# Optimization experiments

Measured on AMD Instinct MI355X. Metric: run time of the kernel, lower is better.

## Reference

```python
import jax, jax.numpy as jnp
import numpy as np

NUM_EXPERTS = 4
HIDDEN = 768
INTER = 192  # expert_inter; gate_up projects to 2*INTER
TOKENS = 131072


def setup_inputs() -> dict:
    key = jax.random.key(0)
    k1, k2, k3, k4 = jax.random.split(key, 4)
    hidden = jax.random.normal(k1, (TOKENS, HIDDEN), dtype=jnp.float32)
    expert_ids = jax.random.randint(k2, (TOKENS,), 0, NUM_EXPERTS, dtype=jnp.int64)
    gate_up = jax.random.normal(k3, (NUM_EXPERTS, HIDDEN, 2 * INTER), dtype=jnp.float32) * 0.02
    down = jax.random.normal(k4, (NUM_EXPERTS, INTER, HIDDEN), dtype=jnp.float32) * 0.02
    return {"hidden": hidden, "expert_ids": expert_ids, "gate_up": gate_up, "down": down}


def reference(hidden, expert_ids, gate_up, down):
    # Math-equivalent to scatter -> per-expert SwiGLU MLP -> gather back:
    # for each token t with expert e = expert_ids[t]:
    #   out[t] = (silu(x_t @ gate_up[e][:, :F]) * (x_t @ gate_up[e][:, F:])) @ down[e]
    # With E=4 (small), compute per-expert dense and select via one-hot; this is
    # jit-friendly (static shapes) and exactly matches the per-token math.
    E = gate_up.shape[0]
    F = down.shape[1]
    onehot = (expert_ids[None, :] == jnp.arange(E)[:, None]).astype(hidden.dtype)  # [E, T]
    gu = jnp.einsum('th,ehf->etf', hidden, gate_up)      # [E, T, 2F]
    gate, up = gu[..., :F], gu[..., F:]                  # [E, T, F]
    act = jax.nn.silu(gate) * up                         # SwiGLU
    out = jnp.einsum('etf,efh,et->th', act, down, onehot)  # select token's own expert
    return out
```

## Files before the change

### kernel.cpp

```cpp
#include <hip/hip_runtime.h>
#include <hip/hip_bf16.h>

#define NE 4
#define HD 768
#define F2 384
#define F1 192
#define NT 131072
#define TT 128

typedef __attribute__((ext_vector_type(8))) short bf16x8;
typedef __attribute__((ext_vector_type(4))) float f32x4;
typedef __attribute__((ext_vector_type(4))) unsigned int u32x4;

#define SMEM_BYTES 123392
#define LTOK 122880u

#define WS_BUCKET_OFF 256
#define WS_B1IMG_OFF (WS_BUCKET_OFF + NE*NT*4)
#define WS_DNIMG_OFF (WS_B1IMG_OFF + NE*24*24576)

__device__ __forceinline__ unsigned short f2bf(float x) {
    unsigned int u = __float_as_uint(x);
    return (unsigned short)((u + 0x7fffu + ((u >> 16) & 1u)) >> 16);
}
__device__ __forceinline__ unsigned int pk2(float a, float b) {
    unsigned int ua = __float_as_uint(a), ub = __float_as_uint(b);
    unsigned int lo = (ua + 0x7fffu + ((ua >> 16) & 1u)) >> 16;
    unsigned int hi = (ub + 0x7fffu + ((ub >> 16) & 1u)) & 0xffff0000u;
    return lo | hi;
}
#define GLL(srcp, ldsoff) \
    __builtin_amdgcn_global_load_lds((const __attribute__((address_space(1))) void*)(srcp), \
        (__attribute__((address_space(3))) void*)(smem + (ldsoff)), 16, 0, 0)

__global__ void route_kernel(const int* __restrict__ ids, int* __restrict__ counts,
                             int* __restrict__ bucket) {
    __shared__ int lc[NE];
    __shared__ int lb[NE];
    int tid = threadIdx.x;
    if (tid < NE) lc[tid] = 0;
    __syncthreads();
    int t = blockIdx.x * blockDim.x + tid;
    int e = ids[t];
    int rank = atomicAdd(&lc[e], 1);
    __syncthreads();
    if (tid < NE) lb[tid] = atomicAdd(&counts[tid], lc[tid]);
    __syncthreads();
    bucket[e * NT + lb[e] + rank] = t;
}

__global__ void b1img_kernel(const float* __restrict__ gu, unsigned short* __restrict__ b1img) {
    int idx = blockIdx.x * 256 + threadIdx.x;
    int L = idx % 1536;
    int es = idx / 1536;
    int kstep = es % 24, e = es / 24;
    int colp = L >> 3, slot = L & 7;
    int v = slot ^ (colp & 7);
    int tc = colp * 2 + (v >> 2);
    int kb = kstep * 32 + (v & 3) * 8;
    const float* src = gu + ((size_t)(e * HD + kb)) * F2 + tc;
    unsigned short o[8];
    #pragma unroll
    for (int j = 0; j < 8; ++j) o[j] = f2bf(src[(size_t)j * F2]);
    *(bf16x8*)(b1img + ((size_t)idx) * 8) = *(const bf16x8*)o;
}

__global__ void dnimg_kernel(const float* __restrict__ dn, unsigned short* __restrict__ dnimg) {
    int idx = blockIdx.x * 256 + threadIdx.x;
    int L = idx % 1536;
    int r = idx / 1536;
    int kt = r % 6; r /= 6;
    int half = r & 1; int e = r >> 1;
    int colp = L >> 3, slot = L & 7;
    int v = slot ^ (colp & 7);
    int tc = colp * 2 + (v >> 2);
    int kb = kt * 32 + (v & 3) * 8;
    const float* src = dn + ((size_t)(e * F1 + kb)) * HD + half * 384 + tc;
    unsigned short o[8];
    #pragma unroll
    for (int j = 0; j < 8; ++j) o[j] = f2bf(src[(size_t)j * HD]);
    *(bf16x8*)(dnimg + ((size_t)idx) * 8) = *(const bf16x8*)o;
}

__global__ __launch_bounds__(512, 1)
void moe_kernel(const float* __restrict__ hidden, const int* __restrict__ counts,
                const int* __restrict__ bucket, const unsigned short* __restrict__ b1img,
                const unsigned short* __restrict__ dnimg, float* __restrict__ out)
{
    extern __shared__ __align__(16) unsigned char smem[];
    const unsigned LAo[2] = {0u, 8192u};
    const unsigned LBo[4] = {16384u, 40960u, 65536u, 90112u};
    const unsigned LCo[3] = {49152u, 73728u, 98304u};
    const unsigned LACT = 0u;

    int rem = blockIdx.x, e, n_e = 0;
    for (e = 0; e < NE; ++e) {
        n_e = counts[e];
        int ntiles = (n_e + TT - 1) >> 7;
        if (rem < ntiles) break;
        rem -= ntiles;
    }
    if (e >= NE) return;
    int t0 = rem << 7;

    int tid = threadIdx.x;
    int lane = tid & 63;
    int w = tid >> 6;
    int rw64 = (w >> 2) << 6;
    int cq = w & 3;
    int lg = lane >> 4;
    int l16 = lane & 15;

    int* tokp = (int*)(smem + LTOK);
    if (tid < TT) {
        int idx = t0 + tid; if (idx >= n_e) idx = n_e - 1;
        tokp[tid] = bucket[e * NT + idx];
    }
    __syncthreads();

    int arow = tid >> 2, kq = tid & 3;
    const float* aptr = hidden + (size_t)tokp[arow] * HD + kq * 8;
    unsigned awb = (unsigned)((tid >> 3) * 128 +
                   (((kq + ((arow & 1) << 2)) ^ ((tid >> 3) & 7)) << 4));

    const unsigned short* gls  = b1img + (size_t)e * 24 * 12288 + (w * 3) * 512 + lane * 8;
    const unsigned short* gls2 = dnimg + (size_t)e * 12 * 12288 + (w * 3) * 512 + lane * 8;
    unsigned gld = (unsigned)(w * 3) * 1024u;

    unsigned laneoff = (unsigned)(((l16 >> 1) << 7) +
                       (((lg + ((l16 & 1) << 2)) ^ (l16 >> 1)) << 4));
    unsigned arb[4], brb[6], b2rb[6];
    #pragma unroll
    for (int mt = 0; mt < 4; ++mt)
        arb[mt] = (unsigned)((rw64 + mt * 16) * 64) + laneoff;
    #pragma unroll
    for (int nt = 0; nt < 6; ++nt) {
        int tcb = (nt < 3) ? (cq * 48 + nt * 16) : (192 + cq * 48 + (nt - 3) * 16);
        brb[nt] = (unsigned)(tcb * 64) + laneoff;
        b2rb[nt] = (unsigned)((cq * 96 + nt * 16) * 64) + laneoff;
    }

    f32x4 avb[4][2];
    const f32x4 fzero = {0.f, 0.f, 0.f, 0.f};
    f32x4 acc[4][6];
    #pragma unroll
    for (int mt = 0; mt < 4; ++mt)
        #pragma unroll
        for (int nt = 0; nt < 6; ++nt) acc[mt][nt] = fzero;

    {
        #pragma unroll
        for (int i = 0; i < 3; ++i) GLL(gls + i * 512, LBo[0] + gld + i * 1024u);
        #pragma unroll
        for (int j = 0; j < 4; ++j) {
            const f32x4* p = (const f32x4*)(aptr + j * 32);
            avb[j][0] = p[0]; avb[j][1] = p[1];
        }
        #pragma unroll
        for (int i = 0; i < 3; ++i) GLL(gls + 12288 + i * 512, LBo[1] + gld + i * 1024u);
        #pragma unroll
        for (int i = 0; i < 3; ++i) GLL(gls + 2 * 12288 + i * 512, LBo[2] + gld + i * 1024u);
        u32x4 vv = {pk2(avb[0][0].x,avb[0][0].y), pk2(avb[0][0].z,avb[0][0].w),
                    pk2(avb[0][1].x,avb[0][1].y), pk2(avb[0][1].z,avb[0][1].w)};
        *(u32x4*)(smem + LAo[0] + awb) = vv;
        asm volatile("s_waitcnt vmcnt(14) lgkmcnt(0)");
        __builtin_amdgcn_s_barrier();
        __builtin_amdgcn_sched_barrier(0);
    }

    #pragma unroll
    for (int g = 0; g < 24; ++g) {
        if (g < 21) {
            #pragma unroll
            for (int i = 0; i < 3; ++i)
                GLL(gls + (size_t)(g + 3) * 12288 + i * 512, LBo[(g + 3) & 3] + gld + i * 1024u);
        }
        if (g < 20) {
            const f32x4* p = (const f32x4*)(aptr + (g + 4) * 32);
            avb[g & 3][0] = p[0]; avb[g & 3][1] = p[1];
        }

        bf16x8 Af[4];
        #pragma unroll
        for (int mt = 0; mt < 4; ++mt)
            Af[mt] = *(const bf16x8*)(smem + LAo[g & 1] + arb[mt]);
        __builtin_amdgcn_s_setprio(1);
        #pragma unroll
        for (int nt = 0; nt < 6; ++nt) {
            bf16x8 Bf = *(const bf16x8*)(smem + LBo[g & 3] + brb[nt]);
            #pragma unroll
            for (int mt = 0; mt < 4; ++mt)
                acc[mt][nt] = __builtin_amdgcn_mfma_f32_16x16x32_bf16(Af[mt], Bf, acc[mt][nt], 0, 0, 0);
        }
        __builtin_amdgcn_s_setprio(0);

        if (g < 23) {
            f32x4 a0 = avb[(g + 1) & 3][0], a1 = avb[(g + 1) & 3][1];
            u32x4 vv = {pk2(a0.x,a0.y), pk2(a0.z,a0.w), pk2(a1.x,a1.y), pk2(a1.z,a1.w)};
            *(u32x4*)(smem + LAo[(g + 1) & 1] + awb) = vv;
            if (g == 0)       asm volatile("s_waitcnt vmcnt(8) lgkmcnt(0)");
            else if (g == 1)  asm volatile("s_waitcnt vmcnt(10) lgkmcnt(0)");
            else if (g <= 19) asm volatile("s_waitcnt vmcnt(12) lgkmcnt(0)");
            else if (g == 20) asm volatile("s_waitcnt vmcnt(10) lgkmcnt(0)");
            else if (g == 21) asm volatile("s_waitcnt vmcnt(5) lgkmcnt(0)");
            else              asm volatile("s_waitcnt vmcnt(0) lgkmcnt(0)");
            __builtin_amdgcn_s_barrier();
            __builtin_amdgcn_sched_barrier(0);
        }
    }

    asm volatile("s_waitcnt vmcnt(0) lgkmcnt(0)");
    __builtin_amdgcn_s_barrier();
    __builtin_amdgcn_sched_barrier(0);

    #pragma unroll
    for (int i = 0; i < 3; ++i) GLL(gls2 + i * 512, LCo[0] + gld + i * 1024u);
    #pragma unroll
    for (int i = 0; i < 3; ++i) GLL(gls2 + 12288 + i * 512, LCo[1] + gld + i * 1024u);

    #pragma unroll
    for (int mt = 0; mt < 4; ++mt)
        #pragma unroll
        for (int nt = 0; nt < 3; ++nt)
            #pragma unroll
            for (int p = 0; p < 4; ++p) {
                float g = acc[mt][nt][p];
                float u = acc[mt][nt + 3][p];
                float s = g / (1.f + __expf(-g));
                int row = rw64 + mt * 16 + 4 * lg + p;
                int f = cq * 48 + nt * 16 + l16;
                int c = f >> 3;
                unsigned b = (unsigned)(LACT + row * 384 + (((c & 24) | ((c & 7) ^ (row & 7))) << 4) + (f & 7) * 2);
                *(unsigned short*)(smem + b) = f2bf(s * u);
            }
    asm volatile("s_waitcnt vmcnt(3) lgkmcnt(0)");
    __builtin_amdgcn_s_barrier();
    __builtin_amdgcn_sched_barrier(0);

    #pragma unroll
    for (int half = 0; half < 2; ++half) {
        f32x4 c2[4][6];
        #pragma unroll
        for (int mt = 0; mt < 4; ++mt)
            #pragma unroll
            for (int nt = 0; nt < 6; ++nt) c2[mt][nt] = fzero;

        #pragma unroll
        for (int kt = 0; kt < 6; ++kt) {
            const int s = half * 6 + kt;
            if (s < 10) {
                #pragma unroll
                for (int i = 0; i < 3; ++i)
                    GLL(gls2 + (size_t)(s + 2) * 12288 + i * 512, LCo[(s + 2) % 3] + gld + i * 1024u);
            }

            int c = kt * 4 + lg;
            unsigned a2sl = (unsigned)(((c & 24) | ((c & 7) ^ (l16 & 7))) << 4);
            bf16x8 A2[4];
            #pragma unroll
            for (int mt = 0; mt < 4; ++mt)
                A2[mt] = *(const bf16x8*)(smem + LACT + (rw64 + mt * 16 + l16) * 384 + a2sl);
            __builtin_amdgcn_s_setprio(1);
            #pragma unroll
            for (int nt = 0; nt < 6; ++nt) {
                bf16x8 B2f = *(const bf16x8*)(smem + LCo[s % 3] + b2rb[nt]);
                #pragma unroll
                for (int mt = 0; mt < 4; ++mt)
                    c2[mt][nt] = __builtin_amdgcn_mfma_f32_16x16x32_bf16(A2[mt], B2f, c2[mt][nt], 0, 0, 0);
            }
            __builtin_amdgcn_s_setprio(0);

            if (s < 11) {
                if (s < 10) asm volatile("s_waitcnt vmcnt(3) lgkmcnt(0)");
                else        asm volatile("s_waitcnt vmcnt(0) lgkmcnt(0)");
                __builtin_amdgcn_s_barrier();
                __builtin_amdgcn_sched_barrier(0);
            }
        }

        #pragma unroll
        for (int mt = 0; mt < 4; ++mt)
            #pragma unroll
            for (int p = 0; p < 4; ++p) {
                int row = rw64 + mt * 16 + 4 * lg + p;
                if (t0 + row < n_e) {
                    float* orow = out + (size_t)tokp[row] * HD + half * 384 + cq * 96 + l16;
                    #pragma unroll
                    for (int nt = 0; nt < 6; ++nt)
                        orow[nt * 16] = c2[mt][nt][p];
                }
            }
    }
}

extern "C" void kernel_launch(void* const* d_in, const int* in_sizes, int n_in,
                              void* d_out, int out_size, void* d_ws, size_t ws_size,
                              hipStream_t stream) {
    (void)in_sizes; (void)n_in; (void)out_size; (void)ws_size;
    const float* hidden = (const float*)d_in[0];
    const int*   ids    = (const int*)d_in[1];
    const float* gu     = (const float*)d_in[2];
    const float* dn     = (const float*)d_in[3];
    float* out = (float*)d_out;

    char* ws = (char*)d_ws;
    int* counts = (int*)ws;
    int* bucket = (int*)(ws + WS_BUCKET_OFF);
    unsigned short* b1img = (unsigned short*)(ws + WS_B1IMG_OFF);
    unsigned short* dnimg = (unsigned short*)(ws + WS_DNIMG_OFF);

    hipMemsetAsync(d_ws, 0, 64, stream);
    route_kernel<<<NT / 256, 256, 0, stream>>>(ids, counts, bucket);
    b1img_kernel<<<576, 256, 0, stream>>>(gu, b1img);
    dnimg_kernel<<<288, 256, 0, stream>>>(dn, dnimg);
    moe_kernel<<<1028, 512, SMEM_BYTES, stream>>>(hidden, counts, bucket, b1img, dnimg, out);
}
```

Before: 283.5 us.

## Shrink LDS buffering to fit two workgroups per CU

Cuts the gate_up weight ring from four LDS stages to two and the down weight ring from three to a single buffer. LDS use drops from about 123 KB to about 74 KB, and launch bounds ask for two 512-thread blocks per CU. The aim is to hide memory latency through occupancy rather than deep software prefetch. In exchange the prefetch distance shrinks to one stage, the waits become tighter, and the down GEMM adds an extra barrier per k-step. Register pressure is also capped by the doubled occupancy target, which may cause spills with the large accumulator arrays.

```diff
diff --git a/kernel.cpp b/kernel.cpp
--- a/kernel.cpp
+++ b/kernel.cpp
@@ -12,8 +12,8 @@
 typedef __attribute__((ext_vector_type(4))) float f32x4;
 typedef __attribute__((ext_vector_type(4))) unsigned int u32x4;
 
-#define SMEM_BYTES 123392
-#define LTOK 122880u
+#define SMEM_BYTES 73984
+#define LTOK 73728u
 
 #define WS_BUCKET_OFF 256
 #define WS_B1IMG_OFF (WS_BUCKET_OFF + NE*NT*4)
@@ -82,15 +82,15 @@
     *(bf16x8*)(dnimg + ((size_t)idx) * 8) = *(const bf16x8*)o;
 }
 
-__global__ __launch_bounds__(512, 1)
+__global__ __launch_bounds__(512, 2)
 void moe_kernel(const float* __restrict__ hidden, const int* __restrict__ counts,
                 const int* __restrict__ bucket, const unsigned short* __restrict__ b1img,
                 const unsigned short* __restrict__ dnimg, float* __restrict__ out)
 {
     extern __shared__ __align__(16) unsigned char smem[];
     const unsigned LAo[2] = {0u, 8192u};
-    const unsigned LBo[4] = {16384u, 40960u, 65536u, 90112u};
-    const unsigned LCo[3] = {49152u, 73728u, 98304u};
+    const unsigned LBo[2] = {16384u, 40960u};
+    const unsigned LB2 = 49152u;
     const unsigned LACT = 0u;
 
     int rem = blockIdx.x, e, n_e = 0;
@@ -137,7 +137,7 @@
     for (int nt = 0; nt < 6; ++nt) {
         int tcb = (nt < 3) ? (cq * 48 + nt * 16) : (192 + cq * 48 + (nt - 3) * 16);
         brb[nt] = (unsigned)(tcb * 64) + laneoff;
-        b2rb[nt] = (unsigned)((cq * 96 + nt * 16) * 64) + laneoff;
+        b2rb[nt] = LB2 + (unsigned)((cq * 96 + nt * 16) * 64) + laneoff;
     }
 
     f32x4 avb[4][2];
@@ -156,24 +156,20 @@
             const f32x4* p = (const f32x4*)(aptr + j * 32);
             avb[j][0] = p[0]; avb[j][1] = p[1];
         }
-        #pragma unroll
-        for (int i = 0; i < 3; ++i) GLL(gls + 12288 + i * 512, LBo[1] + gld + i * 1024u);
-        #pragma unroll
-        for (int i = 0; i < 3; ++i) GLL(gls + 2 * 12288 + i * 512, LBo[2] + gld + i * 1024u);
         u32x4 vv = {pk2(avb[0][0].x,avb[0][0].y), pk2(avb[0][0].z,avb[0][0].w),
                     pk2(avb[0][1].x,avb[0][1].y), pk2(avb[0][1].z,avb[0][1].w)};
         *(u32x4*)(smem + LAo[0] + awb) = vv;
-        asm volatile("s_waitcnt vmcnt(14) lgkmcnt(0)");
+        asm volatile("s_waitcnt vmcnt(3) lgkmcnt(0)");
         __builtin_amdgcn_s_barrier();
         __builtin_amdgcn_sched_barrier(0);
     }
 
     #pragma unroll
     for (int g = 0; g < 24; ++g) {
-        if (g < 21) {
+        if (g < 23) {
             #pragma unroll
             for (int i = 0; i < 3; ++i)
-                GLL(gls + (size_t)(g + 3) * 12288 + i * 512, LBo[(g + 3) & 3] + gld + i * 1024u);
+                GLL(gls + (size_t)(g + 1) * 12288 + i * 512, LBo[(g + 1) & 1] + gld + i * 1024u);
         }
         if (g < 20) {
             const f32x4* p = (const f32x4*)(aptr + (g + 4) * 32);
@@ -187,7 +183,7 @@
         __builtin_amdgcn_s_setprio(1);
         #pragma unroll
         for (int nt = 0; nt < 6; ++nt) {
-            bf16x8 Bf = *(const bf16x8*)(smem + LBo[g & 3] + brb[nt]);
+            bf16x8 Bf = *(const bf16x8*)(smem + LBo[g & 1] + brb[nt]);
             #pragma unroll
             for (int mt = 0; mt < 4; ++mt)
                 acc[mt][nt] = __builtin_amdgcn_mfma_f32_16x16x32_bf16(Af[mt], Bf, acc[mt][nt], 0, 0, 0);
@@ -198,12 +194,8 @@
             f32x4 a0 = avb[(g + 1) & 3][0], a1 = avb[(g + 1) & 3][1];
             u32x4 vv = {pk2(a0.x,a0.y), pk2(a0.z,a0.w), pk2(a1.x,a1.y), pk2(a1.z,a1.w)};
             *(u32x4*)(smem + LAo[(g + 1) & 1] + awb) = vv;
-            if (g == 0)       asm volatile("s_waitcnt vmcnt(8) lgkmcnt(0)");
-            else if (g == 1)  asm volatile("s_waitcnt vmcnt(10) lgkmcnt(0)");
-            else if (g <= 19) asm volatile("s_waitcnt vmcnt(12) lgkmcnt(0)");
-            else if (g == 20) asm volatile("s_waitcnt vmcnt(10) lgkmcnt(0)");
-            else if (g == 21) asm volatile("s_waitcnt vmcnt(5) lgkmcnt(0)");
-            else              asm volatile("s_waitcnt vmcnt(0) lgkmcnt(0)");
+            if (g < 20) asm volatile("s_waitcnt vmcnt(1) lgkmcnt(0)");
+            else        asm volatile("s_waitcnt vmcnt(0) lgkmcnt(0)");
             __builtin_amdgcn_s_barrier();
             __builtin_amdgcn_sched_barrier(0);
         }
@@ -214,9 +206,7 @@
     __builtin_amdgcn_sched_barrier(0);
 
     #pragma unroll
-    for (int i = 0; i < 3; ++i) GLL(gls2 + i * 512, LCo[0] + gld + i * 1024u);
-    #pragma unroll
-    for (int i = 0; i < 3; ++i) GLL(gls2 + 12288 + i * 512, LCo[1] + gld + i * 1024u);
+    for (int i = 0; i < 3; ++i) GLL(gls2 + i * 512, LB2 + gld + i * 1024u);
 
     #pragma unroll
     for (int mt = 0; mt < 4; ++mt)
@@ -233,7 +223,7 @@
                 unsigned b = (unsigned)(LACT + row * 384 + (((c & 24) | ((c & 7) ^ (row & 7))) << 4) + (f & 7) * 2);
                 *(unsigned short*)(smem + b) = f2bf(s * u);
             }
-    asm volatile("s_waitcnt vmcnt(3) lgkmcnt(0)");
+    asm volatile("s_waitcnt vmcnt(0) lgkmcnt(0)");
     __builtin_amdgcn_s_barrier();
     __builtin_amdgcn_sched_barrier(0);
 
@@ -248,31 +238,36 @@
         #pragma unroll
         for (int kt = 0; kt < 6; ++kt) {
             const int s = half * 6 + kt;
-            if (s < 10) {
+
+            int c = kt * 4 + lg;
+            unsigned a2sl = (unsigned)(((c & 24) | ((c & 7) ^ (l16 & 7))) << 4);
+            bf16x8 A2[4], B2f[6];
+            #pragma unroll
+            for (int mt = 0; mt < 4; ++mt)
+                A2[mt] = *(const bf16x8*)(smem + LACT + (rw64 + mt * 16 + l16) * 384 + a2sl);
+            #pragma unroll
+            for (int nt = 0; nt < 6; ++nt)
+                B2f[nt] = *(const bf16x8*)(smem + b2rb[nt]);
+            asm volatile("s_waitcnt lgkmcnt(0)");
+            __builtin_amdgcn_s_barrier();
+            __builtin_amdgcn_sched_barrier(0);
+
+            if (s < 11) {
                 #pragma unroll
                 for (int i = 0; i < 3; ++i)
-                    GLL(gls2 + (size_t)(s + 2) * 12288 + i * 512, LCo[(s + 2) % 3] + gld + i * 1024u);
+                    GLL(gls2 + (size_t)(s + 1) * 12288 + i * 512, LB2 + gld + i * 1024u);
             }
 
-            int c = kt * 4 + lg;
-            unsigned a2sl = (unsigned)(((c & 24) | ((c & 7) ^ (l16 & 7))) << 4);
-            bf16x8 A2[4];
-            #pragma unroll
-            for (int mt = 0; mt < 4; ++mt)
-                A2[mt] = *(const bf16x8*)(smem + LACT + (rw64 + mt * 16 + l16) * 384 + a2sl);
             __builtin_amdgcn_s_setprio(1);
             #pragma unroll
-            for (int nt = 0; nt < 6; ++nt) {
-                bf16x8 B2f = *(const bf16x8*)(smem + LCo[s % 3] + b2rb[nt]);
+            for (int nt = 0; nt < 6; ++nt)
                 #pragma unroll
                 for (int mt = 0; mt < 4; ++mt)
-                    c2[mt][nt] = __builtin_amdgcn_mfma_f32_16x16x32_bf16(A2[mt], B2f, c2[mt][nt], 0, 0, 0);
-            }
+                    c2[mt][nt] = __builtin_amdgcn_mfma_f32_16x16x32_bf16(A2[mt], B2f[nt], c2[mt][nt], 0, 0, 0);
             __builtin_amdgcn_s_setprio(0);
 
             if (s < 11) {
-                if (s < 10) asm volatile("s_waitcnt vmcnt(3) lgkmcnt(0)");
-                else        asm volatile("s_waitcnt vmcnt(0) lgkmcnt(0)");
+                asm volatile("s_waitcnt vmcnt(0)");
                 __builtin_amdgcn_s_barrier();
                 __builtin_amdgcn_sched_barrier(0);
             }
```

Result: slower. 310.1 us (+9.4%).
